# Performance work log

Measured on AMD Instinct MI355X. Metric: run time of the kernel, lower is better.

The kernel has to match this reference:

```python
import jax, jax.numpy as jnp
import numpy as np

# --- static index structures for the 8x8 board ---
_Dic = [[0,0],[0,1],[0,2],[0,3],[1,1],[1,2],[1,3],[2,2],[2,3],[3,3]]
_M = np.zeros((8,8), dtype=np.int32)  # param index for each board cell (4-fold reflective + transpose symmetry)
for _i, (_a, _b) in enumerate(_Dic):
    for _x, _y in [(_a,_b),(7-_a,_b),(_a,7-_b),(7-_a,7-_b)]:
        _M[_x,_y] = _i; _M[_y,_x] = _i
_xs, _ys = np.meshgrid(np.arange(8), np.arange(8), indexing='ij')
# main diagonal id i: cells with y-x=i (i<=7) or x-y=i-7 (i>7)
_main_id = np.where(_ys >= _xs, _ys - _xs, _xs - _ys + 7).reshape(-1)
# anti diagonal id i: cells with x+y=i
_anti_id = (_xs + _ys).reshape(-1)
_main_oh = jnp.asarray((np.arange(15)[None,:] == _main_id[:,None]).astype(np.float32))  # [64,15]
_anti_oh = jnp.asarray((np.arange(15)[None,:] == _anti_id[:,None]).astype(np.float32))  # [64,15]
_Mj = jnp.asarray(_M)


def setup_inputs() -> dict:
    key = jax.random.key(0)
    ks = jax.random.split(key, 11)
    B = 65536
    return {
        'state_input': jax.random.normal(ks[0], (B, 2, 8, 8), dtype=jnp.float32),
        'my_params':  jax.random.uniform(ks[1], (3, 10), dtype=jnp.float32),
        'his_params': jax.random.uniform(ks[2], (3, 10), dtype=jnp.float32),
        'w_act1': jax.random.normal(ks[3], (100, 276), dtype=jnp.float32) * 0.06,
        'b_act1': jax.random.normal(ks[4], (100,), dtype=jnp.float32) * 0.01,
        'w_act2': jax.random.normal(ks[5], (64, 100), dtype=jnp.float32) * 0.1,
        'b_act2': jax.random.normal(ks[6], (64,), dtype=jnp.float32) * 0.01,
        'w_val1': jax.random.normal(ks[7], (64, 276), dtype=jnp.float32) * 0.06,
        'b_val1': jax.random.normal(ks[8], (64,), dtype=jnp.float32) * 0.01,
        'w_val2': jax.random.normal(ks[9], (1, 64), dtype=jnp.float32) * 0.12,
        'b_val2': jax.random.normal(ks[10], (1,), dtype=jnp.float32) * 0.01,
    }


def _my_conv(state_input, my_params, his_params):
    B = state_input.shape[0]
    C = my_params.shape[0]  # 3 channels
    # D[p, j, x, y]: symmetric filter built from 10 params per plane/channel
    D = jnp.stack([my_params, his_params])[:, :, _Mj]  # [2, C, 8, 8]
    # row dots: final order is (channel j, row i, plane p)
    rows = jnp.einsum('bpiy,pjiy->bjip', state_input, D)  # [B, C, 8, 2]
    # col dots: dot(input[b,p,:,i], D[p,j,i,:])
    cols = jnp.einsum('bpxi,pjix->bjip', state_input, D)  # [B, C, 8, 2]
    # elementwise products for diagonal sums
    P = jnp.einsum('bpxy,pjxy->bjpxy', state_input, D).reshape(B, C, 2, 64)
    main = jnp.einsum('bjpn,nk->bjkp', P, _main_oh)  # [B, C, 15, 2]
    anti = jnp.einsum('bjpn,nk->bjkp', P, _anti_oh)  # [B, C, 15, 2]
    return jnp.concatenate([rows.reshape(B, -1), cols.reshape(B, -1),
                            main.reshape(B, -1), anti.reshape(B, -1)], axis=1)  # [B, 276]


def reference(state_input, my_params, his_params,
              w_act1, b_act1, w_act2, b_act2,
              w_val1, b_val1, w_val2, b_val2):
    x = jax.nn.relu(_my_conv(state_input, my_params, his_params))
    x_act = jax.nn.relu(x @ w_act1.T + b_act1)
    x_act = jax.nn.log_softmax(x_act @ w_act2.T + b_act2, axis=-1)  # [B, 64]
    x_val = jax.nn.relu(x @ w_val1.T + b_val1)
    x_val = jnp.tanh(x_val @ w_val2.T + b_val2)  # [B, 1]
    return (x_act, x_val)
```

## Files before the change

### kernel.cpp

```cpp
#include <hip/hip_runtime.h>

typedef float f32x4 __attribute__((ext_vector_type(4)));
typedef short bf16x8 __attribute__((ext_vector_type(8)));

__device__ __forceinline__ short f2bf(float f) {
    union { float f; unsigned u; } c; c.f = f;
    unsigned r = (c.u + 0x7fffu + ((c.u >> 16) & 1u)) >> 16;
    return (short)r;
}

#define XT_S 296
#define AY_S 136
#define ZL_S 68

#define DEXT_SHORTS (18*4*512)
#define W1_SHORTS   (99*512)
#define W2_SHORTS   (16*512)
#define WS2_SHORTS  (DEXT_SHORTS + W1_SHORTS + W2_SHORTS)

__device__ __forceinline__ int m8(int x, int y) {
    constexpr int M8[8][8] = {
        {0,1,2,3,3,2,1,0},{1,4,5,6,6,5,4,1},{2,5,7,8,8,7,5,2},{3,6,8,9,9,8,6,3},
        {3,6,8,9,9,8,6,3},{2,5,7,8,8,7,5,2},{1,4,5,6,6,5,4,1},{0,1,2,3,3,2,1,0}};
    return M8[x][y];
}

__global__ __launch_bounds__(256) void prep2(
    const float* __restrict__ myp,  const float* __restrict__ hisp,
    const float* __restrict__ w1a,  const float* __restrict__ w1v,
    const float* __restrict__ w2a,  short* __restrict__ ws)
{
    int i = blockIdx.x * 256 + threadIdx.x;
    if (i >= WS2_SHORTS) return;
    float v = 0.f;
    if (i < DEXT_SHORTS) {
        int e = i & 7, lane = (i >> 3) & 63, tc = i >> 9;
        int nt = tc >> 2, kc = tc & 3;
        int n = nt * 16 + (lane & 15);
        int k = kc * 32 + (lane >> 4) * 8 + e;
        int p = k >> 6, cell = k & 63, x = cell >> 3, y = cell & 7;
        const float* pr = p ? hisp : myp;
        if (n < 276) {
            bool match = false; int j = 0;
            if (n < 48)       { int p2 = n & 1, t = n >> 1; j = t >> 3; match = (p2 == p) && ((t & 7) == x); }
            else if (n < 96)  { int m = n - 48, p2 = m & 1, t = m >> 1; j = t >> 3; match = (p2 == p) && ((t & 7) == y); }
            else if (n < 186) { int m = n - 96, p2 = m & 1, t = m >> 1; j = t / 15;
                                match = (p2 == p) && ((t % 15) == ((y >= x) ? (y - x) : (x - y + 7))); }
            else              { int m = n - 186, p2 = m & 1, t = m >> 1; j = t / 15;
                                match = (p2 == p) && ((t % 15) == (x + y)); }
            if (match) v = pr[j * 10 + m8(x, y)];
        }
    } else if (i < DEXT_SHORTS + W1_SHORTS) {
        int ii = i - DEXT_SHORTS;
        int e = ii & 7, lane = (ii >> 3) & 63, tc = ii >> 9;
        int nt = tc / 9, kc = tc % 9;
        int n = nt * 16 + (lane & 15);
        int k = kc * 32 + (lane >> 4) * 8 + e;
        if (k < 276) {
            if (n < 100)                  v = w1a[n * 276 + k];
            else if (n >= 112 && n < 176) v = w1v[(n - 112) * 276 + k];
        }
    } else {
        int ii = i - DEXT_SHORTS - W1_SHORTS;
        int e = ii & 7, lane = (ii >> 3) & 63, tc = ii >> 9;
        int n = (tc >> 2) * 16 + (lane & 15);
        int k = (tc & 3) * 32 + (lane >> 4) * 8 + e;
        if (k < 100) v = w2a[n * 100 + k];
    }
    ws[i] = f2bf(v);
}

__global__ __launch_bounds__(384) void net_v5(
    const float* __restrict__ state,
    const float* __restrict__ b1a, const float* __restrict__ b2a,
    const float* __restrict__ b1v, const float* __restrict__ w2v,
    const float* __restrict__ b2v,
    const short* __restrict__ ws, float* __restrict__ out, int Btot)
{
    __shared__ __align__(16) unsigned char smem[28160];
    short* xt   = (short*)smem;
    float* zl   = (float*)smem;
    short* ay   = (short*)(smem + 18944);
    float* valp = (float*)(smem + 27648);

    const int tid  = threadIdx.x;
    const int w    = tid >> 6;
    const int l    = tid & 63;
    const int lrow = l & 15;
    const int lk   = l >> 4;
    const int bg0  = blockIdx.x * 32;

    {
        const float* sp = state + (size_t)bg0 * 128;
        #pragma unroll
        for (int it = 0; it < 3; ++it) {
            int t = tid + it * 384;
            if (t < 1024) {
                f32x4 v4 = *(const f32x4*)(sp + t * 4);
                int f = t * 4, row = f >> 7, col = f & 127;
                short* dst = ay + row * AY_S + col;
                dst[0] = f2bf(v4[0]); dst[1] = f2bf(v4[1]);
                dst[2] = f2bf(v4[2]); dst[3] = f2bf(v4[3]);
            }
        }
    }
    bf16x8 dx0[4], dx1[4], dx2[4];
    #pragma unroll
    for (int kc = 0; kc < 4; ++kc) {
        dx0[kc] = *(const bf16x8*)(ws + (((w     ) * 4 + kc) * 64 + l) * 8);
        dx1[kc] = *(const bf16x8*)(ws + (((w +  6) * 4 + kc) * 64 + l) * 8);
        dx2[kc] = *(const bf16x8*)(ws + (((w + 12) * 4 + kc) * 64 + l) * 8);
    }
    __syncthreads();

    {
        f32x4 c0[2], c1[2], c2[2];
        #pragma unroll
        for (int mt = 0; mt < 2; ++mt) {
            c0[mt] = (f32x4){0.f,0.f,0.f,0.f};
            c1[mt] = (f32x4){0.f,0.f,0.f,0.f};
            c2[mt] = (f32x4){0.f,0.f,0.f,0.f};
        }
        #pragma unroll
        for (int mt = 0; mt < 2; ++mt) {
            bf16x8 a[4];
            #pragma unroll
            for (int kc = 0; kc < 4; ++kc)
                a[kc] = *(const bf16x8*)(ay + (mt * 16 + lrow) * AY_S + kc * 32 + lk * 8);
            #pragma unroll
            for (int kc = 0; kc < 4; ++kc) {
                c0[mt] = __builtin_amdgcn_mfma_f32_16x16x32_bf16(a[kc], dx0[kc], c0[mt], 0, 0, 0);
                c1[mt] = __builtin_amdgcn_mfma_f32_16x16x32_bf16(a[kc], dx1[kc], c1[mt], 0, 0, 0);
                c2[mt] = __builtin_amdgcn_mfma_f32_16x16x32_bf16(a[kc], dx2[kc], c2[mt], 0, 0, 0);
            }
        }
        #pragma unroll
        for (int mt = 0; mt < 2; ++mt)
            #pragma unroll
            for (int r = 0; r < 4; ++r) {
                short* xr = xt + (mt * 16 + lk * 4 + r) * XT_S + lrow;
                xr[(w     ) * 16] = f2bf(fmaxf(c0[mt][r], 0.f));
                xr[(w +  6) * 16] = f2bf(fmaxf(c1[mt][r], 0.f));
                xr[(w + 12) * 16] = f2bf(fmaxf(c2[mt][r], 0.f));
            }
    }
    const bool haveB = (w < 5);
    bf16x8 bfA[9], bfB[9];
    #pragma unroll
    for (int kc = 0; kc < 9; ++kc)
        bfA[kc] = *(const bf16x8*)(ws + DEXT_SHORTS + ((w * 9 + kc) * 64 + l) * 8);
    if (haveB) {
        #pragma unroll
        for (int kc = 0; kc < 9; ++kc)
            bfB[kc] = *(const bf16x8*)(ws + DEXT_SHORTS + (((w + 6) * 9 + kc) * 64 + l) * 8);
    }
    float epbA, epbB = 0.f, epwB = 0.f;
    { const int colA = w * 16 + lrow; epbA = (colA < 100) ? b1a[colA] : 0.f; }
    if (haveB) {
        const int colB = (w + 6) * 16 + lrow;
        if (w == 0) epbB = (colB < 100) ? b1a[colB] : 0.f;
        else { epbB = b1v[colB - 112]; epwB = w2v[colB - 112]; }
    }
    __syncthreads();

    {
        f32x4 accA[2], accB[2];
        #pragma unroll
        for (int mt = 0; mt < 2; ++mt) {
            accA[mt] = (f32x4){0.f,0.f,0.f,0.f};
            accB[mt] = (f32x4){0.f,0.f,0.f,0.f};
        }
        #pragma unroll
        for (int mt = 0; mt < 2; ++mt) {
            bf16x8 a[9];
            #pragma unroll
            for (int kc = 0; kc < 9; ++kc)
                a[kc] = *(const bf16x8*)(xt + (mt * 16 + lrow) * XT_S + kc * 32 + lk * 8);
            #pragma unroll
            for (int kc = 0; kc < 9; ++kc)
                accA[mt] = __builtin_amdgcn_mfma_f32_16x16x32_bf16(a[kc], bfA[kc], accA[mt], 0, 0, 0);
            if (haveB) {
                #pragma unroll
                for (int kc = 0; kc < 9; ++kc)
                    accB[mt] = __builtin_amdgcn_mfma_f32_16x16x32_bf16(a[kc], bfB[kc], accB[mt], 0, 0, 0);
            }
        }
        #pragma unroll
        for (int mt = 0; mt < 2; ++mt)
            #pragma unroll
            for (int r = 0; r < 4; ++r) {
                float v = fmaxf(accA[mt][r] + epbA, 0.f);
                ay[(mt * 16 + lk * 4 + r) * AY_S + w * 16 + lrow] = f2bf(v);
            }
        if (haveB) {
            if (w == 0) {
                #pragma unroll
                for (int mt = 0; mt < 2; ++mt)
                    #pragma unroll
                    for (int r = 0; r < 4; ++r) {
                        const int row = mt * 16 + lk * 4 + r;
                        float v = fmaxf(accB[mt][r] + epbB, 0.f);
                        ay[row * AY_S +  96 + lrow] = f2bf(v);
                        ay[row * AY_S + 112 + lrow] = 0;
                    }
            } else {
                #pragma unroll
                for (int mt = 0; mt < 2; ++mt)
                    #pragma unroll
                    for (int r = 0; r < 4; ++r) {
                        float v = fmaxf(accB[mt][r] + epbB, 0.f) * epwB;
                        v += __shfl_xor(v, 1); v += __shfl_xor(v, 2);
                        v += __shfl_xor(v, 4); v += __shfl_xor(v, 8);
                        if (lrow == 0) valp[(w - 1) * 32 + mt * 16 + lk * 4 + r] = v;
                    }
            }
        }
    }
    bf16x8 b2f[4];
    float bias2 = 0.f;
    if (w < 4) {
        #pragma unroll
        for (int kc = 0; kc < 4; ++kc)
            b2f[kc] = *(const bf16x8*)(ws + DEXT_SHORTS + W1_SHORTS + ((w * 4 + kc) * 64 + l) * 8);
        bias2 = b2a[w * 16 + lrow];
    }
    __syncthreads();

    if (w < 4) {
        f32x4 acc2[2];
        #pragma unroll
        for (int mt = 0; mt < 2; ++mt) acc2[mt] = (f32x4){0.f,0.f,0.f,0.f};
        #pragma unroll
        for (int mt = 0; mt < 2; ++mt)
            #pragma unroll
            for (int kc = 0; kc < 4; ++kc) {
                bf16x8 a2 = *(const bf16x8*)(ay + (mt * 16 + lrow) * AY_S + kc * 32 + lk * 8);
                acc2[mt] = __builtin_amdgcn_mfma_f32_16x16x32_bf16(a2, b2f[kc], acc2[mt], 0, 0, 0);
            }
        #pragma unroll
        for (int mt = 0; mt < 2; ++mt)
            #pragma unroll
            for (int r = 0; r < 4; ++r)
                zl[(mt * 16 + lk * 4 + r) * ZL_S + w * 16 + lrow] = acc2[mt][r] + bias2;
    } else if (w == 5 && l < 32) {
        float v = valp[l] + valp[32 + l] + valp[64 + l] + valp[96 + l] + b2v[0];
        out[(size_t)Btot * 64 + bg0 + l] = tanhf(v);
    }
    __syncthreads();

    if (w < 4) {
        const int rl = l >> 3, q = l & 7;
        const int row = w * 8 + rl;
        const float* zr = zl + row * ZL_S + q * 8;
        f32x4 v0 = *(const f32x4*)(zr);
        f32x4 v1 = *(const f32x4*)(zr + 4);
        float m = fmaxf(fmaxf(fmaxf(v0[0], v0[1]), fmaxf(v0[2], v0[3])),
                        fmaxf(fmaxf(v1[0], v1[1]), fmaxf(v1[2], v1[3])));
        m = fmaxf(m, __shfl_xor(m, 1));
        m = fmaxf(m, __shfl_xor(m, 2));
        m = fmaxf(m, __shfl_xor(m, 4));
        float s = 0.f;
        #pragma unroll
        for (int e = 0; e < 4; ++e) s += __expf(v0[e] - m);
        #pragma unroll
        for (int e = 0; e < 4; ++e) s += __expf(v1[e] - m);
        s += __shfl_xor(s, 1);
        s += __shfl_xor(s, 2);
        s += __shfl_xor(s, 4);
        const float lsm = m + __logf(s);
        #pragma unroll
        for (int i = 0; i < 2; ++i) {
            const int rloc  = i * 4 + (l >> 4);
            const int row_s = w * 8 + rloc;
            const float lz  = __shfl(lsm, rloc * 8);
            f32x4 zv = *(const f32x4*)(zl + row_s * ZL_S + (l & 15) * 4);
            f32x4 ov;
            #pragma unroll
            for (int e = 0; e < 4; ++e) ov[e] = zv[e] - lz;
            *(f32x4*)(out + (size_t)(bg0 + row_s) * 64 + (l & 15) * 4) = ov;
        }
    }
}

__global__ __launch_bounds__(384) void net_v1(
    const float* __restrict__ state,
    const float* __restrict__ myp,  const float* __restrict__ hisp,
    const float* __restrict__ w1a,  const float* __restrict__ b1a,
    const float* __restrict__ w2a,  const float* __restrict__ b2a,
    const float* __restrict__ w1v,  const float* __restrict__ b1v,
    const float* __restrict__ w2v,  const float* __restrict__ b2v,
    float* __restrict__ out, int Btot)
{
    __shared__ __align__(16) unsigned char smem[56320];
    short* xt   = (short*)smem;
    float* zl   = (float*)smem;
    short* ay   = (short*)(smem + 37888);
    float* valp = (float*)(smem + 55296);
    const int tid = threadIdx.x, w = tid >> 6, l = tid & 63, lrow = l & 15, lk = l >> 4;
    const int bg0 = blockIdx.x * 64;
    const bool haveB = (w < 5);

    const int cp = (w >= 3) ? 1 : 0, cj = (w >= 3) ? (w - 3) : w;
    float prm[10];
    { const float* ps = (cp == 0 ? myp : hisp) + cj * 10;
      #pragma unroll
      for (int i = 0; i < 10; i++) prm[i] = ps[i]; }
    for (int i = tid; i < 9472; i += 384) ((unsigned*)xt)[i] = 0u;
    __syncthreads();
    {
        float racc[8], cacc[8], macc[15], aacc[15];
        #pragma unroll
        for (int i = 0; i < 8; i++) { racc[i] = 0.f; cacc[i] = 0.f; }
        #pragma unroll
        for (int i = 0; i < 15; i++) { macc[i] = 0.f; aacc[i] = 0.f; }
        const float* S = state + ((size_t)(bg0 + l) * 2 + cp) * 64;
        #pragma unroll
        for (int x = 0; x < 8; x++) {
            f32x4 lo = *(const f32x4*)(S + x * 8);
            f32x4 hi = *(const f32x4*)(S + x * 8 + 4);
            #pragma unroll
            for (int y = 0; y < 8; y++) {
                float s = (y < 4) ? lo[y] : hi[y - 4];
                float t = s * prm[m8(x, y)];
                racc[x] += t; cacc[y] += t;
                macc[(y >= x) ? (y - x) : (x - y + 7)] += t;
                aacc[x + y] += t;
            }
        }
        short* xr = xt + l * XT_S;
        #pragma unroll
        for (int i = 0; i < 8; i++)  xr[(cj * 8 + i) * 2 + cp]        = f2bf(fmaxf(racc[i], 0.f));
        #pragma unroll
        for (int i = 0; i < 8; i++)  xr[48 + (cj * 8 + i) * 2 + cp]   = f2bf(fmaxf(cacc[i], 0.f));
        #pragma unroll
        for (int k = 0; k < 15; k++) xr[96 + (cj * 15 + k) * 2 + cp]  = f2bf(fmaxf(macc[k], 0.f));
        #pragma unroll
        for (int k = 0; k < 15; k++) xr[186 + (cj * 15 + k) * 2 + cp] = f2bf(fmaxf(aacc[k], 0.f));
    }
    bf16x8 bfA[9], bfB[9];
    {
        const int nA = w * 16 + lrow;
        const float* srcA = (nA < 100) ? (w1a + (size_t)nA * 276) : w1a;
        #pragma unroll
        for (int kc = 0; kc < 9; kc++) {
            bf16x8 r;
            #pragma unroll
            for (int e = 0; e < 8; e++) {
                int k = kc * 32 + lk * 8 + e;
                bool ok = (nA < 100) && (k < 276);
                r[e] = f2bf(ok ? srcA[k] : 0.f);
            }
            bfA[kc] = r;
        }
        if (haveB) {
            const int nB = (w + 6) * 16 + lrow;
            const float* srcB; bool validB;
            if (nB < 100)       { srcB = w1a + (size_t)nB * 276;         validB = true; }
            else if (nB >= 112) { srcB = w1v + (size_t)(nB - 112) * 276; validB = true; }
            else                { srcB = w1a;                            validB = false; }
            #pragma unroll
            for (int kc = 0; kc < 9; kc++) {
                bf16x8 r;
                #pragma unroll
                for (int e = 0; e < 8; e++) {
                    int k = kc * 32 + lk * 8 + e;
                    bool ok = validB && (k < 276);
                    r[e] = f2bf(ok ? srcB[k] : 0.f);
                }
                bfB[kc] = r;
            }
        }
    }
    float epbA, epbB = 0.f, epwB = 0.f;
    { const int colA = w * 16 + lrow; epbA = (colA < 100) ? b1a[colA] : 0.f; }
    if (haveB) {
        const int colB = (w + 6) * 16 + lrow;
        if (w == 0) epbB = (colB < 100) ? b1a[colB] : 0.f;
        else { epbB = b1v[colB - 112]; epwB = w2v[colB - 112]; }
    }
    __syncthreads();
    {
        f32x4 accA[4], accB[4];
        #pragma unroll
        for (int mt = 0; mt < 4; ++mt) {
            accA[mt] = (f32x4){0.f,0.f,0.f,0.f};
            accB[mt] = (f32x4){0.f,0.f,0.f,0.f};
        }
        #pragma unroll
        for (int mt = 0; mt < 4; ++mt) {
            bf16x8 a[9];
            #pragma unroll
            for (int kc = 0; kc < 9; ++kc)
                a[kc] = *(const bf16x8*)(xt + (mt * 16 + lrow) * XT_S + kc * 32 + lk * 8);
            #pragma unroll
            for (int kc = 0; kc < 9; ++kc)
                accA[mt] = __builtin_amdgcn_mfma_f32_16x16x32_bf16(a[kc], bfA[kc], accA[mt], 0, 0, 0);
            if (haveB) {
                #pragma unroll
                for (int kc = 0; kc < 9; ++kc)
                    accB[mt] = __builtin_amdgcn_mfma_f32_16x16x32_bf16(a[kc], bfB[kc], accB[mt], 0, 0, 0);
            }
        }
        #pragma unroll
        for (int mt = 0; mt < 4; ++mt)
            #pragma unroll
            for (int r = 0; r < 4; ++r) {
                float v = fmaxf(accA[mt][r] + epbA, 0.f);
                ay[(mt * 16 + lk * 4 + r) * AY_S + w * 16 + lrow] = f2bf(v);
            }
        if (haveB) {
            if (w == 0) {
                #pragma unroll
                for (int mt = 0; mt < 4; ++mt)
                    #pragma unroll
                    for (int r = 0; r < 4; ++r) {
                        const int row = mt * 16 + lk * 4 + r;
                        float v = fmaxf(accB[mt][r] + epbB, 0.f);
                        ay[row * AY_S +  96 + lrow] = f2bf(v);
                        ay[row * AY_S + 112 + lrow] = 0;
                    }
            } else {
                #pragma unroll
                for (int mt = 0; mt < 4; ++mt)
                    #pragma unroll
                    for (int r = 0; r < 4; ++r) {
                        float v = fmaxf(accB[mt][r] + epbB, 0.f) * epwB;
                        v += __shfl_xor(v, 1); v += __shfl_xor(v, 2);
                        v += __shfl_xor(v, 4); v += __shfl_xor(v, 8);
                        if (lrow == 0) valp[(w - 1) * 64 + mt * 16 + lk * 4 + r] = v;
                    }
            }
        }
    }
    bf16x8 b2f[4];
    float bias2 = 0.f;
    if (w < 4) {
        const float* src2 = w2a + (size_t)(w * 16 + lrow) * 100;
        #pragma unroll
        for (int kc = 0; kc < 4; kc++) {
            bf16x8 r;
            #pragma unroll
            for (int e = 0; e < 8; e++) { int k = kc * 32 + lk * 8 + e; r[e] = f2bf((k < 100) ? src2[k] : 0.f); }
            b2f[kc] = r;
        }
        bias2 = b2a[w * 16 + lrow];
    }
    __syncthreads();
    if (w < 4) {
        f32x4 acc2[4];
        #pragma unroll
        for (int mt = 0; mt < 4; ++mt) acc2[mt] = (f32x4){0.f,0.f,0.f,0.f};
        #pragma unroll
        for (int mt = 0; mt < 4; ++mt)
            #pragma unroll
            for (int kc = 0; kc < 4; ++kc) {
                bf16x8 a2 = *(const bf16x8*)(ay + (mt * 16 + lrow) * AY_S + kc * 32 + lk * 8);
                acc2[mt] = __builtin_amdgcn_mfma_f32_16x16x32_bf16(a2, b2f[kc], acc2[mt], 0, 0, 0);
            }
        #pragma unroll
        for (int mt = 0; mt < 4; ++mt)
            #pragma unroll
            for (int r = 0; r < 4; ++r)
                zl[(mt * 16 + lk * 4 + r) * ZL_S + w * 16 + lrow] = acc2[mt][r] + bias2;
    } else if (w == 5) {
        float v = valp[l] + valp[64 + l] + valp[128 + l] + valp[192 + l] + b2v[0];
        out[(size_t)Btot * 64 + bg0 + l] = tanhf(v);
    }
    __syncthreads();
    if (w < 4) {
        const int rl = l >> 2, q = l & 3;
        const int row = w * 16 + rl;
        const float* zr = zl + row * ZL_S;
        f32x4 v[4]; float m = -1e30f;
        #pragma unroll
        for (int c = 0; c < 4; ++c) {
            v[c] = *(const f32x4*)(zr + c * 16 + q * 4);
            m = fmaxf(m, fmaxf(fmaxf(v[c][0], v[c][1]), fmaxf(v[c][2], v[c][3])));
        }
        m = fmaxf(m, __shfl_xor(m, 1));
        m = fmaxf(m, __shfl_xor(m, 2));
        float s = 0.f;
        #pragma unroll
        for (int c = 0; c < 4; ++c)
            #pragma unroll
            for (int e = 0; e < 4; ++e) s += __expf(v[c][e] - m);
        s += __shfl_xor(s, 1);
        s += __shfl_xor(s, 2);
        const float lsm = m + __logf(s);
        float* o = out + (size_t)(bg0 + row) * 64;
        #pragma unroll
        for (int c = 0; c < 4; ++c) {
            f32x4 ov;
            #pragma unroll
            for (int e = 0; e < 4; ++e) ov[e] = v[c][e] - lsm;
            *(f32x4*)(o + c * 16 + q * 4) = ov;
        }
    }
}

extern "C" void kernel_launch(void* const* d_in, const int* in_sizes, int n_in,
                              void* d_out, int out_size, void* d_ws, size_t ws_size,
                              hipStream_t stream) {
    const float* state = (const float*)d_in[0];
    const float* myp   = (const float*)d_in[1];
    const float* hisp  = (const float*)d_in[2];
    const float* w1a   = (const float*)d_in[3];
    const float* b1a   = (const float*)d_in[4];
    const float* w2a   = (const float*)d_in[5];
    const float* b2a   = (const float*)d_in[6];
    const float* w1v   = (const float*)d_in[7];
    const float* b1v   = (const float*)d_in[8];
    const float* w2v   = (const float*)d_in[9];
    const float* b2v   = (const float*)d_in[10];
    float* out = (float*)d_out;
    const int Btot = in_sizes[0] / 128;
    if (ws_size >= (size_t)WS2_SHORTS * sizeof(short)) {
        short* ws = (short*)d_ws;
        prep2<<<dim3((WS2_SHORTS + 255) / 256), dim3(256), 0, stream>>>(myp, hisp, w1a, w1v, w2a, ws);
        net_v5<<<dim3(Btot / 32), dim3(384), 0, stream>>>(
            state, b1a, b2a, b1v, w2v, b2v, ws, out, Btot);
    } else {
        net_v1<<<dim3(Btot / 64), dim3(384), 0, stream>>>(
            state, myp, hisp, w1a, b1a, w2a, b2a, w1v, b1v, w2v, b2v, out, Btot);
    }
}
```

Measured before the change: 53.25 us.

## Restructure fused net so each wave owns 16 rows with transposed MFMA and folded biases

Replaces the block-cooperative kernel, in which waves split output columns across 32 rows with several block barriers, with a per-wave design. Each wave processes 16 batch rows end to end, loading its state directly into registers. It uses weights as the MFMA A operand streamed from global or L2, and keeps activations in a private LDS slice, so no __syncthreads is needed. Biases are folded into the GEMMs through an appended ones column, and the value head and log-softmax become in-register shuffle reductions. The cost is that every wave re-reads the full weight set from cache, and register pressure rises from 18+11 accumulator tiles.

```diff
diff --git a/kernel.cpp b/kernel.cpp
--- a/kernel.cpp
+++ b/kernel.cpp
@@ -8,10 +8,13 @@
     unsigned r = (c.u + 0x7fffu + ((c.u >> 16) & 1u)) >> 16;
     return (short)r;
 }
-
-#define XT_S 296
-#define AY_S 136
-#define ZL_S 68
+__device__ __forceinline__ unsigned pk2(float a, float b) {
+    return (unsigned)(unsigned short)f2bf(a) | ((unsigned)(unsigned short)f2bf(b) << 16);
+}
+
+#define XROW 296
+#define YROW 136
+#define WLDS 4736
 
 #define DEXT_SHORTS (18*4*512)
 #define W1_SHORTS   (99*512)
@@ -28,7 +31,9 @@
 __global__ __launch_bounds__(256) void prep2(
     const float* __restrict__ myp,  const float* __restrict__ hisp,
     const float* __restrict__ w1a,  const float* __restrict__ w1v,
-    const float* __restrict__ w2a,  short* __restrict__ ws)
+    const float* __restrict__ w2a,  const float* __restrict__ b1a,
+    const float* __restrict__ b1v,  const float* __restrict__ b2a,
+    short* __restrict__ ws)
 {
     int i = blockIdx.x * 256 + threadIdx.x;
     if (i >= WS2_SHORTS) return;
@@ -59,226 +64,139 @@
         if (k < 276) {
             if (n < 100)                  v = w1a[n * 276 + k];
             else if (n >= 112 && n < 176) v = w1v[(n - 112) * 276 + k];
+        } else if (k == 276) {
+            if (n < 100)                  v = b1a[n];
+            else if (n >= 112 && n < 176) v = b1v[n - 112];
         }
     } else {
         int ii = i - DEXT_SHORTS - W1_SHORTS;
         int e = ii & 7, lane = (ii >> 3) & 63, tc = ii >> 9;
         int n = (tc >> 2) * 16 + (lane & 15);
         int k = (tc & 3) * 32 + (lane >> 4) * 8 + e;
-        if (k < 100) v = w2a[n * 100 + k];
+        if (k < 100)       v = w2a[n * 100 + k];
+        else if (k == 112) v = b2a[n];
     }
     ws[i] = f2bf(v);
 }
 
-__global__ __launch_bounds__(384) void net_v5(
+__global__ __launch_bounds__(256) void net_v6(
     const float* __restrict__ state,
-    const float* __restrict__ b1a, const float* __restrict__ b2a,
-    const float* __restrict__ b1v, const float* __restrict__ w2v,
-    const float* __restrict__ b2v,
+    const float* __restrict__ w2v_, const float* __restrict__ b2v_,
     const short* __restrict__ ws, float* __restrict__ out, int Btot)
 {
-    __shared__ __align__(16) unsigned char smem[28160];
-    short* xt   = (short*)smem;
-    float* zl   = (float*)smem;
-    short* ay   = (short*)(smem + 18944);
-    float* valp = (float*)(smem + 27648);
-
-    const int tid  = threadIdx.x;
-    const int w    = tid >> 6;
-    const int l    = tid & 63;
-    const int lrow = l & 15;
-    const int lk   = l >> 4;
-    const int bg0  = blockIdx.x * 32;
-
+    __shared__ __align__(16) short smem[4 * WLDS];
+    const int tid = threadIdx.x;
+    const int w   = tid >> 6;
+    const int l   = tid & 63;
+    const int lq  = l >> 4;
+    const int lr  = l & 15;
+    const int bg  = blockIdx.x * 64 + w * 16;
+    short* X = smem + w * WLDS;
+
+    const float wv   = w2v_[l];
+    const float b2v0 = b2v_[0];
+
+    bf16x8 sf[4];
     {
-        const float* sp = state + (size_t)bg0 * 128;
-        #pragma unroll
-        for (int it = 0; it < 3; ++it) {
-            int t = tid + it * 384;
-            if (t < 1024) {
-                f32x4 v4 = *(const f32x4*)(sp + t * 4);
-                int f = t * 4, row = f >> 7, col = f & 127;
-                short* dst = ay + row * AY_S + col;
-                dst[0] = f2bf(v4[0]); dst[1] = f2bf(v4[1]);
-                dst[2] = f2bf(v4[2]); dst[3] = f2bf(v4[3]);
-            }
-        }
-    }
-    bf16x8 dx0[4], dx1[4], dx2[4];
-    #pragma unroll
-    for (int kc = 0; kc < 4; ++kc) {
-        dx0[kc] = *(const bf16x8*)(ws + (((w     ) * 4 + kc) * 64 + l) * 8);
-        dx1[kc] = *(const bf16x8*)(ws + (((w +  6) * 4 + kc) * 64 + l) * 8);
-        dx2[kc] = *(const bf16x8*)(ws + (((w + 12) * 4 + kc) * 64 + l) * 8);
-    }
-    __syncthreads();
+        const float* sp = state + (size_t)(bg + lr) * 128 + lq * 8;
+        #pragma unroll
+        for (int kc = 0; kc < 4; ++kc) {
+            f32x4 lo = *(const f32x4*)(sp + kc * 32);
+            f32x4 hi = *(const f32x4*)(sp + kc * 32 + 4);
+            bf16x8 r;
+            #pragma unroll
+            for (int e = 0; e < 4; ++e) { r[e] = f2bf(lo[e]); r[4 + e] = f2bf(hi[e]); }
+            sf[kc] = r;
+        }
+    }
+
+    f32x4 c1[18];
+    #pragma unroll
+    for (int nt = 0; nt < 18; ++nt) c1[nt] = (f32x4){0.f,0.f,0.f,0.f};
+    #pragma unroll
+    for (int nt = 0; nt < 18; ++nt)
+        #pragma unroll
+        for (int kc = 0; kc < 4; ++kc) {
+            bf16x8 a = *(const bf16x8*)(ws + ((nt * 4 + kc) * 64 + l) * 8);
+            c1[nt] = __builtin_amdgcn_mfma_f32_16x16x32_bf16(a, sf[kc], c1[nt], 0, 0, 0);
+        }
+    #pragma unroll
+    for (int nt = 0; nt < 18; ++nt) {
+        unsigned* d = (unsigned*)(X + lr * XROW + nt * 16 + lq * 4);
+        d[0] = pk2(fmaxf(c1[nt][0], 0.f), fmaxf(c1[nt][1], 0.f));
+        d[1] = pk2(fmaxf(c1[nt][2], 0.f), fmaxf(c1[nt][3], 0.f));
+    }
+    if (l < 16) X[l * XROW + 276] = (short)0x3F80;
+
+    bf16x8 xf[9];
+    #pragma unroll
+    for (int kc = 0; kc < 9; ++kc)
+        xf[kc] = *(const bf16x8*)(X + lr * XROW + kc * 32 + lq * 8);
+
+    f32x4 a2[11];
+    #pragma unroll
+    for (int nt = 0; nt < 11; ++nt) a2[nt] = (f32x4){0.f,0.f,0.f,0.f};
+    #pragma unroll
+    for (int nt = 0; nt < 11; ++nt)
+        #pragma unroll
+        for (int kc = 0; kc < 9; ++kc) {
+            bf16x8 wa = *(const bf16x8*)(ws + DEXT_SHORTS + ((nt * 9 + kc) * 64 + l) * 8);
+            a2[nt] = __builtin_amdgcn_mfma_f32_16x16x32_bf16(wa, xf[kc], a2[nt], 0, 0, 0);
+        }
+
+    *(unsigned long long*)(X + (l >> 2) * YROW + 112 + (l & 3) * 4) = 0ULL;
+    #pragma unroll
+    for (int nt = 0; nt < 7; ++nt) {
+        unsigned* d = (unsigned*)(X + lr * YROW + nt * 16 + lq * 4);
+        d[0] = pk2(fmaxf(a2[nt][0], 0.f), fmaxf(a2[nt][1], 0.f));
+        d[1] = pk2(fmaxf(a2[nt][2], 0.f), fmaxf(a2[nt][3], 0.f));
+    }
+    if (l < 16) X[l * YROW + 112] = (short)0x3F80;
 
     {
-        f32x4 c0[2], c1[2], c2[2];
-        #pragma unroll
-        for (int mt = 0; mt < 2; ++mt) {
-            c0[mt] = (f32x4){0.f,0.f,0.f,0.f};
-            c1[mt] = (f32x4){0.f,0.f,0.f,0.f};
-            c2[mt] = (f32x4){0.f,0.f,0.f,0.f};
-        }
-        #pragma unroll
-        for (int mt = 0; mt < 2; ++mt) {
-            bf16x8 a[4];
-            #pragma unroll
-            for (int kc = 0; kc < 4; ++kc)
-                a[kc] = *(const bf16x8*)(ay + (mt * 16 + lrow) * AY_S + kc * 32 + lk * 8);
-            #pragma unroll
-            for (int kc = 0; kc < 4; ++kc) {
-                c0[mt] = __builtin_amdgcn_mfma_f32_16x16x32_bf16(a[kc], dx0[kc], c0[mt], 0, 0, 0);
-                c1[mt] = __builtin_amdgcn_mfma_f32_16x16x32_bf16(a[kc], dx1[kc], c1[mt], 0, 0, 0);
-                c2[mt] = __builtin_amdgcn_mfma_f32_16x16x32_bf16(a[kc], dx2[kc], c2[mt], 0, 0, 0);
-            }
-        }
-        #pragma unroll
-        for (int mt = 0; mt < 2; ++mt)
-            #pragma unroll
-            for (int r = 0; r < 4; ++r) {
-                short* xr = xt + (mt * 16 + lk * 4 + r) * XT_S + lrow;
-                xr[(w     ) * 16] = f2bf(fmaxf(c0[mt][r], 0.f));
-                xr[(w +  6) * 16] = f2bf(fmaxf(c1[mt][r], 0.f));
-                xr[(w + 12) * 16] = f2bf(fmaxf(c2[mt][r], 0.f));
-            }
-    }
-    const bool haveB = (w < 5);
-    bf16x8 bfA[9], bfB[9];
-    #pragma unroll
-    for (int kc = 0; kc < 9; ++kc)
-        bfA[kc] = *(const bf16x8*)(ws + DEXT_SHORTS + ((w * 9 + kc) * 64 + l) * 8);
-    if (haveB) {
-        #pragma unroll
-        for (int kc = 0; kc < 9; ++kc)
-            bfB[kc] = *(const bf16x8*)(ws + DEXT_SHORTS + (((w + 6) * 9 + kc) * 64 + l) * 8);
-    }
-    float epbA, epbB = 0.f, epwB = 0.f;
-    { const int colA = w * 16 + lrow; epbA = (colA < 100) ? b1a[colA] : 0.f; }
-    if (haveB) {
-        const int colB = (w + 6) * 16 + lrow;
-        if (w == 0) epbB = (colB < 100) ? b1a[colB] : 0.f;
-        else { epbB = b1v[colB - 112]; epwB = w2v[colB - 112]; }
-    }
-    __syncthreads();
-
-    {
-        f32x4 accA[2], accB[2];
-        #pragma unroll
-        for (int mt = 0; mt < 2; ++mt) {
-            accA[mt] = (f32x4){0.f,0.f,0.f,0.f};
-            accB[mt] = (f32x4){0.f,0.f,0.f,0.f};
-        }
-        #pragma unroll
-        for (int mt = 0; mt < 2; ++mt) {
-            bf16x8 a[9];
-            #pragma unroll
-            for (int kc = 0; kc < 9; ++kc)
-                a[kc] = *(const bf16x8*)(xt + (mt * 16 + lrow) * XT_S + kc * 32 + lk * 8);
-            #pragma unroll
-            for (int kc = 0; kc < 9; ++kc)
-                accA[mt] = __builtin_amdgcn_mfma_f32_16x16x32_bf16(a[kc], bfA[kc], accA[mt], 0, 0, 0);
-            if (haveB) {
-                #pragma unroll
-                for (int kc = 0; kc < 9; ++kc)
-                    accB[mt] = __builtin_amdgcn_mfma_f32_16x16x32_bf16(a[kc], bfB[kc], accB[mt], 0, 0, 0);
-            }
-        }
-        #pragma unroll
-        for (int mt = 0; mt < 2; ++mt)
-            #pragma unroll
-            for (int r = 0; r < 4; ++r) {
-                float v = fmaxf(accA[mt][r] + epbA, 0.f);
-                ay[(mt * 16 + lk * 4 + r) * AY_S + w * 16 + lrow] = f2bf(v);
-            }
-        if (haveB) {
-            if (w == 0) {
-                #pragma unroll
-                for (int mt = 0; mt < 2; ++mt)
-                    #pragma unroll
-                    for (int r = 0; r < 4; ++r) {
-                        const int row = mt * 16 + lk * 4 + r;
-                        float v = fmaxf(accB[mt][r] + epbB, 0.f);
-                        ay[row * AY_S +  96 + lrow] = f2bf(v);
-                        ay[row * AY_S + 112 + lrow] = 0;
-                    }
-            } else {
-                #pragma unroll
-                for (int mt = 0; mt < 2; ++mt)
-                    #pragma unroll
-                    for (int r = 0; r < 4; ++r) {
-                        float v = fmaxf(accB[mt][r] + epbB, 0.f) * epwB;
-                        v += __shfl_xor(v, 1); v += __shfl_xor(v, 2);
-                        v += __shfl_xor(v, 4); v += __shfl_xor(v, 8);
-                        if (lrow == 0) valp[(w - 1) * 32 + mt * 16 + lk * 4 + r] = v;
-                    }
-            }
-        }
-    }
-    bf16x8 b2f[4];
-    float bias2 = 0.f;
-    if (w < 4) {
-        #pragma unroll
-        for (int kc = 0; kc < 4; ++kc)
-            b2f[kc] = *(const bf16x8*)(ws + DEXT_SHORTS + W1_SHORTS + ((w * 4 + kc) * 64 + l) * 8);
-        bias2 = b2a[w * 16 + lrow];
-    }
-    __syncthreads();
-
-    if (w < 4) {
-        f32x4 acc2[2];
-        #pragma unroll
-        for (int mt = 0; mt < 2; ++mt) acc2[mt] = (f32x4){0.f,0.f,0.f,0.f};
-        #pragma unroll
-        for (int mt = 0; mt < 2; ++mt)
-            #pragma unroll
-            for (int kc = 0; kc < 4; ++kc) {
-                bf16x8 a2 = *(const bf16x8*)(ay + (mt * 16 + lrow) * AY_S + kc * 32 + lk * 8);
-                acc2[mt] = __builtin_amdgcn_mfma_f32_16x16x32_bf16(a2, b2f[kc], acc2[mt], 0, 0, 0);
-            }
-        #pragma unroll
-        for (int mt = 0; mt < 2; ++mt)
+        float vs = 0.f;
+        #pragma unroll
+        for (int nt = 7; nt < 11; ++nt)
             #pragma unroll
             for (int r = 0; r < 4; ++r)
-                zl[(mt * 16 + lk * 4 + r) * ZL_S + w * 16 + lrow] = acc2[mt][r] + bias2;
-    } else if (w == 5 && l < 32) {
-        float v = valp[l] + valp[32 + l] + valp[64 + l] + valp[96 + l] + b2v[0];
-        out[(size_t)Btot * 64 + bg0 + l] = tanhf(v);
-    }
-    __syncthreads();
-
-    if (w < 4) {
-        const int rl = l >> 3, q = l & 7;
-        const int row = w * 8 + rl;
-        const float* zr = zl + row * ZL_S + q * 8;
-        f32x4 v0 = *(const f32x4*)(zr);
-        f32x4 v1 = *(const f32x4*)(zr + 4);
-        float m = fmaxf(fmaxf(fmaxf(v0[0], v0[1]), fmaxf(v0[2], v0[3])),
-                        fmaxf(fmaxf(v1[0], v1[1]), fmaxf(v1[2], v1[3])));
+                vs += fmaxf(a2[nt][r], 0.f) * __shfl(wv, (nt - 7) * 16 + lq * 4 + r);
+        vs += __shfl_xor(vs, 16);
+        vs += __shfl_xor(vs, 32);
+        if (l < 16) out[(size_t)Btot * 64 + bg + l] = tanhf(vs + b2v0);
+    }
+
+    bf16x8 yf[4];
+    #pragma unroll
+    for (int kc = 0; kc < 4; ++kc)
+        yf[kc] = *(const bf16x8*)(X + lr * YROW + kc * 32 + lq * 8);
+    f32x4 z[4];
+    #pragma unroll
+    for (int nt = 0; nt < 4; ++nt) z[nt] = (f32x4){0.f,0.f,0.f,0.f};
+    #pragma unroll
+    for (int nt = 0; nt < 4; ++nt)
+        #pragma unroll
+        for (int kc = 0; kc < 4; ++kc) {
+            bf16x8 wb = *(const bf16x8*)(ws + DEXT_SHORTS + W1_SHORTS + ((nt * 4 + kc) * 64 + l) * 8);
+            z[nt] = __builtin_amdgcn_mfma_f32_16x16x32_bf16(yf[kc], wb, z[nt], 0, 0, 0);
+        }
+
+    #pragma unroll
+    for (int r = 0; r < 4; ++r) {
+        float m = fmaxf(fmaxf(z[0][r], z[1][r]), fmaxf(z[2][r], z[3][r]));
         m = fmaxf(m, __shfl_xor(m, 1));
         m = fmaxf(m, __shfl_xor(m, 2));
         m = fmaxf(m, __shfl_xor(m, 4));
-        float s = 0.f;
-        #pragma unroll
-        for (int e = 0; e < 4; ++e) s += __expf(v0[e] - m);
-        #pragma unroll
-        for (int e = 0; e < 4; ++e) s += __expf(v1[e] - m);
+        m = fmaxf(m, __shfl_xor(m, 8));
+        float s = __expf(z[0][r] - m) + __expf(z[1][r] - m)
+                + __expf(z[2][r] - m) + __expf(z[3][r] - m);
         s += __shfl_xor(s, 1);
         s += __shfl_xor(s, 2);
         s += __shfl_xor(s, 4);
+        s += __shfl_xor(s, 8);
         const float lsm = m + __logf(s);
-        #pragma unroll
-        for (int i = 0; i < 2; ++i) {
-            const int rloc  = i * 4 + (l >> 4);
-            const int row_s = w * 8 + rloc;
-            const float lz  = __shfl(lsm, rloc * 8);
-            f32x4 zv = *(const f32x4*)(zl + row_s * ZL_S + (l & 15) * 4);
-            f32x4 ov;
-            #pragma unroll
-            for (int e = 0; e < 4; ++e) ov[e] = zv[e] - lz;
-            *(f32x4*)(out + (size_t)(bg0 + row_s) * 64 + (l & 15) * 4) = ov;
-        }
+        float* o = out + (size_t)(bg + lq * 4 + r) * 64 + lr;
+        #pragma unroll
+        for (int nt = 0; nt < 4; ++nt) o[nt * 16] = z[nt][r] - lsm;
     }
 }
 
@@ -299,7 +217,6 @@
     const int tid = threadIdx.x, w = tid >> 6, l = tid & 63, lrow = l & 15, lk = l >> 4;
     const int bg0 = blockIdx.x * 64;
     const bool haveB = (w < 5);
-
     const int cp = (w >= 3) ? 1 : 0, cj = (w >= 3) ? (w - 3) : w;
     float prm[10];
     { const float* ps = (cp == 0 ? myp : hisp) + cj * 10;
@@ -327,7 +244,7 @@
                 aacc[x + y] += t;
             }
         }
-        short* xr = xt + l * XT_S;
+        short* xr = xt + l * XROW;
         #pragma unroll
         for (int i = 0; i < 8; i++)  xr[(cj * 8 + i) * 2 + cp]        = f2bf(fmaxf(racc[i], 0.f));
         #pragma unroll
@@ -391,7 +308,7 @@
             bf16x8 a[9];
             #pragma unroll
             for (int kc = 0; kc < 9; ++kc)
-                a[kc] = *(const bf16x8*)(xt + (mt * 16 + lrow) * XT_S + kc * 32 + lk * 8);
+                a[kc] = *(const bf16x8*)(xt + (mt * 16 + lrow) * XROW + kc * 32 + lk * 8);
             #pragma unroll
             for (int kc = 0; kc < 9; ++kc)
                 accA[mt] = __builtin_amdgcn_mfma_f32_16x16x32_bf16(a[kc], bfA[kc], accA[mt], 0, 0, 0);
@@ -406,7 +323,7 @@
             #pragma unroll
             for (int r = 0; r < 4; ++r) {
                 float v = fmaxf(accA[mt][r] + epbA, 0.f);
-                ay[(mt * 16 + lk * 4 + r) * AY_S + w * 16 + lrow] = f2bf(v);
+                ay[(mt * 16 + lk * 4 + r) * YROW + w * 16 + lrow] = f2bf(v);
             }
         if (haveB) {
             if (w == 0) {
@@ -416,8 +333,8 @@
                     for (int r = 0; r < 4; ++r) {
                         const int row = mt * 16 + lk * 4 + r;
                         float v = fmaxf(accB[mt][r] + epbB, 0.f);
-                        ay[row * AY_S +  96 + lrow] = f2bf(v);
-                        ay[row * AY_S + 112 + lrow] = 0;
+                        ay[row * YROW +  96 + lrow] = f2bf(v);
+                        ay[row * YROW + 112 + lrow] = 0;
                     }
             } else {
                 #pragma unroll
@@ -454,14 +371,14 @@
         for (int mt = 0; mt < 4; ++mt)
             #pragma unroll
             for (int kc = 0; kc < 4; ++kc) {
-                bf16x8 a2 = *(const bf16x8*)(ay + (mt * 16 + lrow) * AY_S + kc * 32 + lk * 8);
-                acc2[mt] = __builtin_amdgcn_mfma_f32_16x16x32_bf16(a2, b2f[kc], acc2[mt], 0, 0, 0);
+                bf16x8 a2v = *(const bf16x8*)(ay + (mt * 16 + lrow) * YROW + kc * 32 + lk * 8);
+                acc2[mt] = __builtin_amdgcn_mfma_f32_16x16x32_bf16(a2v, b2f[kc], acc2[mt], 0, 0, 0);
             }
         #pragma unroll
         for (int mt = 0; mt < 4; ++mt)
             #pragma unroll
             for (int r = 0; r < 4; ++r)
-                zl[(mt * 16 + lk * 4 + r) * ZL_S + w * 16 + lrow] = acc2[mt][r] + bias2;
+                zl[(mt * 16 + lk * 4 + r) * 68 + w * 16 + lrow] = acc2[mt][r] + bias2;
     } else if (w == 5) {
         float v = valp[l] + valp[64 + l] + valp[128 + l] + valp[192 + l] + b2v[0];
         out[(size_t)Btot * 64 + bg0 + l] = tanhf(v);
@@ -470,7 +387,7 @@
     if (w < 4) {
         const int rl = l >> 2, q = l & 3;
         const int row = w * 16 + rl;
-        const float* zr = zl + row * ZL_S;
+        const float* zr = zl + row * 68;
         f32x4 v[4]; float m = -1e30f;
         #pragma unroll
         for (int c = 0; c < 4; ++c) {
@@ -516,9 +433,10 @@
     const int Btot = in_sizes[0] / 128;
     if (ws_size >= (size_t)WS2_SHORTS * sizeof(short)) {
         short* ws = (short*)d_ws;
-        prep2<<<dim3((WS2_SHORTS + 255) / 256), dim3(256), 0, stream>>>(myp, hisp, w1a, w1v, w2a, ws);
-        net_v5<<<dim3(Btot / 32), dim3(384), 0, stream>>>(
-            state, b1a, b2a, b1v, w2v, b2v, ws, out, Btot);
+        prep2<<<dim3((WS2_SHORTS + 255) / 256), dim3(256), 0, stream>>>(
+            myp, hisp, w1a, w1v, w2a, b1a, b1v, b2a, ws);
+        net_v6<<<dim3(Btot / 64), dim3(256), 0, stream>>>(
+            state, w2v, b2v, ws, out, Btot);
     } else {
         net_v1<<<dim3(Btot / 64), dim3(384), 0, stream>>>(
             state, myp, hisp, w1a, b1a, w2a, b2a, w1v, b1v, w2v, b2v, out, Btot);
```

Result: slower. 68.36 us (+28.4%).
